# Kernel tuning notes

Measured on AMD Instinct MI355X. Metric: run time of the kernel, lower is better.

The kernel has to match this reference:

```python
import jax, jax.numpy as jnp
import numpy as np

EPS = 1e-06
LAMBDA_PCSL = 0.1
LAMBDA_GPAL = 0.1


def setup_inputs() -> dict:
    key = jax.random.key(0)
    k1, k2 = jax.random.split(key)
    N, D, P = 262144, 256, 512
    features = jax.random.normal(k1, (N, D), dtype=jnp.float32)
    patient_ids = jax.random.randint(k2, (N,), 0, P, dtype=jnp.int64)
    return {"features": features, "patient_ids": patient_ids, "num_patients": P}


def _pafa_loss(features, patient_ids, num_patients):
    # Segmented mean: centroids[p] = mean of features with patient_ids == p
    seg_ids = patient_ids.astype(jnp.int32)
    sums = jax.ops.segment_sum(features, seg_ids, num_segments=num_patients)  # [P, D]
    counts = jax.ops.segment_sum(jnp.ones((features.shape[0],), features.dtype),
                                 seg_ids, num_segments=num_patients)          # [P]
    counts = jnp.maximum(counts, 1.0)  # every patient assumed present (as in original)
    centroids = sums / counts[:, None]                                        # [P, D]

    # Within-patient variance: sum_i ||x_i - c_{pid_i}||^2
    diff = features - centroids[seg_ids]                                      # [N, D]
    within_variance = jnp.sum(diff * diff)

    # Pairwise centroid distances: sum_{i<j} ||c_i - c_j||^2
    #   = P * sum_i ||c_i||^2 - ||sum_i c_i||^2   (exact identity, no O(P^2) loop)
    sq_norms = jnp.sum(centroids * centroids, axis=1)                         # [P]
    total = jnp.sum(centroids, axis=0)                                        # [D]
    P = jnp.asarray(num_patients, centroids.dtype)
    between_distance = P * jnp.sum(sq_norms) - jnp.sum(total * total)

    loss_pcsl = within_variance / (between_distance + EPS)

    # Global patient alignment: mean ||c_p - mean(c)||^2
    global_centroid = jnp.mean(centroids, axis=0)                             # [D]
    gdiff = centroids - global_centroid
    loss_gpal = jnp.mean(jnp.sum(gdiff * gdiff, axis=1))

    return LAMBDA_PCSL * loss_pcsl + LAMBDA_GPAL * loss_gpal


def reference(features, patient_ids, num_patients):
    return _pafa_loss(features, patient_ids, num_patients)
```

## Files before the change

kernel.cpp:

```cpp
#include <hip/hip_runtime.h>


#define DIMS 256
#define NPAT 512
#define HB 64
#define HT 1024
#define CPAD 16


extern "C" __global__ void __launch_bounds__(HT)
k_hist(const int* __restrict__ pids, int N, unsigned* __restrict__ bh)
{
    __shared__ unsigned h[NPAT];
    const int t = threadIdx.x;
    if (t < NPAT) h[t] = 0u;
    __syncthreads();

    const int r = (blockIdx.x * HT + t) * 4;
    if (r + 3 < N) {
        const int4 p4 = *reinterpret_cast<const int4*>(pids + r);
        atomicAdd(&h[p4.x], 1u);
        atomicAdd(&h[p4.y], 1u);
        atomicAdd(&h[p4.z], 1u);
        atomicAdd(&h[p4.w], 1u);
    } else {
        for (int k = 0; k < 4; ++k)
            if (r + k < N) atomicAdd(&h[pids[r + k]], 1u);
    }
    __syncthreads();
    if (t < NPAT) bh[t * HB + blockIdx.x] = h[t];
}

extern "C" __global__ void __launch_bounds__(NPAT)
k_scan(const unsigned* __restrict__ bh, unsigned* __restrict__ counts,
       unsigned* __restrict__ starts, unsigned* __restrict__ cursor,
       float* __restrict__ scalars, float* __restrict__ T)
{
    __shared__ unsigned tmp[NPAT];
    const int t = threadIdx.x;
    unsigned c = 0u;
    const uint4* row = reinterpret_cast<const uint4*>(bh + t * HB);
    #pragma unroll
    for (int k = 0; k < HB / 4; ++k) {
        const uint4 v = row[k];
        c += v.x + v.y + v.z + v.w;
    }
    counts[t] = c;
    tmp[t] = c;
    __syncthreads();
    for (int off = 1; off < NPAT; off <<= 1) {
        const unsigned v = (t >= off) ? tmp[t - off] : 0u;
        __syncthreads();
        tmp[t] += v;
        __syncthreads();
    }
    const unsigned st = tmp[t] - c;
    starts[t] = st;
    cursor[t * CPAD] = st;
    if (t < 4)    scalars[t] = 0.0f;
    if (t < DIMS) T[t]       = 0.0f;
}

extern "C" __global__ void __launch_bounds__(HT)
k_scatter(const int* __restrict__ pids, int N,
          unsigned* __restrict__ cursor, unsigned* __restrict__ idx)
{
    __shared__ unsigned h[NPAT];
    __shared__ unsigned basec[NPAT];
    __shared__ int      spid[HT * 4];

    const int t = threadIdx.x;
    if (t < NPAT) h[t] = 0u;
    __syncthreads();

    const int r = (blockIdx.x * HT + t) * 4;
    int4 p4 = make_int4(-1, -1, -1, -1);
    if (r + 3 < N) {
        p4 = *reinterpret_cast<const int4*>(pids + r);
        atomicAdd(&h[p4.x], 1u);
        atomicAdd(&h[p4.y], 1u);
        atomicAdd(&h[p4.z], 1u);
        atomicAdd(&h[p4.w], 1u);
    } else {
        if (r + 0 < N) { p4.x = pids[r + 0]; atomicAdd(&h[p4.x], 1u); }
        if (r + 1 < N) { p4.y = pids[r + 1]; atomicAdd(&h[p4.y], 1u); }
        if (r + 2 < N) { p4.z = pids[r + 2]; atomicAdd(&h[p4.z], 1u); }
        if (r + 3 < N) { p4.w = pids[r + 3]; atomicAdd(&h[p4.w], 1u); }
    }
    spid[t * 4 + 0] = p4.x;
    spid[t * 4 + 1] = p4.y;
    spid[t * 4 + 2] = p4.z;
    spid[t * 4 + 3] = p4.w;
    __syncthreads();

    if (t < NPAT) {
        const unsigned hc = h[t];
        basec[t] = hc ? atomicAdd(&cursor[t * CPAD], hc) : 0u;
    }
    __syncthreads();

    #pragma unroll
    for (int k = 0; k < 4; ++k) {
        const int pid = spid[t * 4 + k];
        if (pid >= 0) {
            const unsigned pos = atomicAdd(&basec[pid], 1u);
            idx[pos] = (unsigned)(r + k);
        }
    }
}

extern "C" __global__ void __launch_bounds__(512)
k_main(const float* __restrict__ feats, const unsigned* __restrict__ idx,
       const unsigned* __restrict__ counts, const unsigned* __restrict__ starts,
       float* __restrict__ T, float* __restrict__ scalars)
{
    __shared__ float part[8][DIMS];
    __shared__ float sred[8];
    __shared__ float cred[4];

    const int p    = blockIdx.x;
    const int lane = threadIdx.x & 63;
    const int w    = threadIdx.x >> 6;
    const unsigned start = starts[p];
    const unsigned cnt   = counts[p];
    const unsigned base  = lane * 4;

    float ax = 0.f, ay = 0.f, az = 0.f, aw = 0.f;
    float ssq = 0.f;

    unsigned j = (unsigned)w;
    for (; j + 56 < cnt; j += 64) {
        unsigned rr[8];
        #pragma unroll
        for (int k = 0; k < 8; ++k) rr[k] = idx[start + j + 8 * k];
        float4 v[8];
        #pragma unroll
        for (int k = 0; k < 8; ++k)
            v[k] = *reinterpret_cast<const float4*>(feats + (size_t)rr[k] * DIMS + base);
        #pragma unroll
        for (int k = 0; k < 8; ++k) {
            ax += v[k].x; ay += v[k].y; az += v[k].z; aw += v[k].w;
            ssq += v[k].x*v[k].x + v[k].y*v[k].y + v[k].z*v[k].z + v[k].w*v[k].w;
        }
    }
    for (; j < cnt; j += 8) {
        const unsigned row = idx[start + j];
        const float4 v = *reinterpret_cast<const float4*>(feats + (size_t)row * DIMS + base);
        ax += v.x; ay += v.y; az += v.z; aw += v.w;
        ssq += v.x*v.x + v.y*v.y + v.z*v.z + v.w*v.w;
    }

    part[w][base + 0] = ax;
    part[w][base + 1] = ay;
    part[w][base + 2] = az;
    part[w][base + 3] = aw;
    for (int off = 32; off; off >>= 1) ssq += __shfl_down(ssq, off, 64);
    if (lane == 0) sred[w] = ssq;
    __syncthreads();

    const int d = threadIdx.x;
    if (d < DIMS) {
        float s = 0.f;
        #pragma unroll
        for (int ww = 0; ww < 8; ++ww) s += part[ww][d];
        const float cntf = fmaxf((float)cnt, 1.0f);
        const float c = s / cntf;
        atomicAdd(&T[d], c);
        float csq = c * c;
        for (int off = 32; off; off >>= 1) csq += __shfl_down(csq, off, 64);
        if ((d & 63) == 0) cred[d >> 6] = csq;
    }
    __syncthreads();

    if (threadIdx.x == 0) {
        const float s2p = cred[0] + cred[1] + cred[2] + cred[3];
        const float cntf = fmaxf((float)cnt, 1.0f);
        atomicAdd(&scalars[2], s2p);
        atomicAdd(&scalars[1], cntf * s2p);
        float sq = 0.f;
        #pragma unroll
        for (int ww = 0; ww < 8; ++ww) sq += sred[ww];
        atomicAdd(&scalars[0], sq);
    }
}

extern "C" __global__ void __launch_bounds__(DIMS)
k_final(const float* __restrict__ T, const float* __restrict__ scalars,
        const int* __restrict__ nump, float* __restrict__ out)
{
    __shared__ float red[4];
    const int d = threadIdx.x;
    const float t = T[d];
    float tt = t * t;
    for (int off = 32; off; off >>= 1) tt += __shfl_down(tt, off, 64);
    if ((d & 63) == 0) red[d >> 6] = tt;
    __syncthreads();
    if (d == 0) {
        const double TT    = (double)red[0] + red[1] + red[2] + red[3];
        const double SumSq = (double)scalars[0];
        const double S1    = (double)scalars[1];
        const double S2    = (double)scalars[2];
        const double Pd    = (double)(*nump);
        const double within  = SumSq - S1;
        const double between = Pd * S2 - TT;
        const double pcsl = within / (between + 1e-6);
        const double gpal = S2 / Pd - TT / (Pd * Pd);
        out[0] = (float)(0.1 * pcsl + 0.1 * gpal);
    }
}

extern "C" void kernel_launch(void* const* d_in, const int* in_sizes, int n_in,
                              void* d_out, int out_size, void* d_ws, size_t ws_size,
                              hipStream_t stream)
{
    const float* feats = (const float*)d_in[0];
    const int*   pids  = (const int*)d_in[1];
    const int*   nump  = (const int*)d_in[2];
    float*       out   = (float*)d_out;

    const int N = in_sizes[0] / DIMS;

    char* ws = (char*)d_ws;
    unsigned* counts  = (unsigned*)(ws);
    unsigned* starts  = (unsigned*)(ws + 2048);
    float*    scalars = (float*)(ws + 4096);
    float*    T       = (float*)(ws + 4352);
    unsigned* cursor  = (unsigned*)(ws + 8192);
    unsigned* bh      = (unsigned*)(ws + 40960);
    unsigned* idx     = (unsigned*)(ws + 173056);

    k_hist   <<<dim3(HB),   dim3(HT),   0, stream>>>(pids, N, bh);
    k_scan   <<<dim3(1),    dim3(NPAT), 0, stream>>>(bh, counts, starts, cursor,
                                                     scalars, T);
    k_scatter<<<dim3(HB),   dim3(HT),   0, stream>>>(pids, N, cursor, idx);
    k_main   <<<dim3(NPAT), dim3(512),  0, stream>>>(feats, idx, counts, starts,
                                                     T, scalars);
    k_final  <<<dim3(1),    dim3(DIMS), 0, stream>>>(T, scalars, nump, out);
}
```

Before: 76.88 us.

## Precompute per-block scatter offsets, fold final reduction into main kernel, broadcast row indices

The scan kernel now writes an exclusive prefix of each patient's per-block histogram into that histogram. The scatter kernel can then seed its shared cursors directly from starts plus the per-block offset, with no re-histogram and no global atomics on a padded cursor array. The separate final kernel is removed: the last block of k_main, found through an atomic done counter, computes the loss. In k_main, each warp now takes a contiguous chunk of a patient's rows, loads 64 indices in one coalesced read and broadcasts them with readlane. This cuts one launch and redundant scatter work, at the cost of last-block synchronisation and possibly unbalanced chunks.

Result: slower. 207.7 us (+170.2%).

```diff
diff --git a/kernel.cpp b/kernel.cpp
--- a/kernel.cpp
+++ b/kernel.cpp
@@ -5,7 +5,6 @@
 #define NPAT 512
 #define HB 64
 #define HT 1024
-#define CPAD 16
 
 
 extern "C" __global__ void __launch_bounds__(HT)
@@ -32,21 +31,28 @@
 }
 
 extern "C" __global__ void __launch_bounds__(NPAT)
-k_scan(const unsigned* __restrict__ bh, unsigned* __restrict__ counts,
-       unsigned* __restrict__ starts, unsigned* __restrict__ cursor,
-       float* __restrict__ scalars, float* __restrict__ T)
+k_scan(unsigned* __restrict__ bh, unsigned* __restrict__ counts,
+       unsigned* __restrict__ starts, float* __restrict__ scalars,
+       float* __restrict__ T, unsigned* __restrict__ done)
 {
     __shared__ unsigned tmp[NPAT];
     const int t = threadIdx.x;
-    unsigned c = 0u;
-    const uint4* row = reinterpret_cast<const uint4*>(bh + t * HB);
+
+    uint4* row = reinterpret_cast<uint4*>(bh + t * HB);
+    unsigned run = 0u;
     #pragma unroll
     for (int k = 0; k < HB / 4; ++k) {
         const uint4 v = row[k];
-        c += v.x + v.y + v.z + v.w;
-    }
-    counts[t] = c;
-    tmp[t] = c;
+        uint4 e;
+        e.x = run;
+        e.y = e.x + v.x;
+        e.z = e.y + v.y;
+        e.w = e.z + v.z;
+        run = e.w + v.w;
+        row[k] = e;
+    }
+    counts[t] = run;
+    tmp[t] = run;
     __syncthreads();
     for (int off = 1; off < NPAT; off <<= 1) {
         const unsigned v = (t >= off) ? tmp[t - off] : 0u;
@@ -54,69 +60,49 @@
         tmp[t] += v;
         __syncthreads();
     }
-    const unsigned st = tmp[t] - c;
-    starts[t] = st;
-    cursor[t * CPAD] = st;
+    starts[t] = tmp[t] - run;
+
     if (t < 4)    scalars[t] = 0.0f;
+    if (t == 4)   *done      = 0u;
     if (t < DIMS) T[t]       = 0.0f;
 }
 
 extern "C" __global__ void __launch_bounds__(HT)
 k_scatter(const int* __restrict__ pids, int N,
-          unsigned* __restrict__ cursor, unsigned* __restrict__ idx)
-{
-    __shared__ unsigned h[NPAT];
+          const unsigned* __restrict__ bh, const unsigned* __restrict__ starts,
+          unsigned* __restrict__ idx)
+{
     __shared__ unsigned basec[NPAT];
-    __shared__ int      spid[HT * 4];
-
     const int t = threadIdx.x;
-    if (t < NPAT) h[t] = 0u;
+    if (t < NPAT) basec[t] = starts[t] + bh[t * HB + blockIdx.x];
     __syncthreads();
 
     const int r = (blockIdx.x * HT + t) * 4;
-    int4 p4 = make_int4(-1, -1, -1, -1);
     if (r + 3 < N) {
-        p4 = *reinterpret_cast<const int4*>(pids + r);
-        atomicAdd(&h[p4.x], 1u);
-        atomicAdd(&h[p4.y], 1u);
-        atomicAdd(&h[p4.z], 1u);
-        atomicAdd(&h[p4.w], 1u);
+        const int4 p4 = *reinterpret_cast<const int4*>(pids + r);
+        idx[atomicAdd(&basec[p4.x], 1u)] = (unsigned)(r + 0);
+        idx[atomicAdd(&basec[p4.y], 1u)] = (unsigned)(r + 1);
+        idx[atomicAdd(&basec[p4.z], 1u)] = (unsigned)(r + 2);
+        idx[atomicAdd(&basec[p4.w], 1u)] = (unsigned)(r + 3);
     } else {
-        if (r + 0 < N) { p4.x = pids[r + 0]; atomicAdd(&h[p4.x], 1u); }
-        if (r + 1 < N) { p4.y = pids[r + 1]; atomicAdd(&h[p4.y], 1u); }
-        if (r + 2 < N) { p4.z = pids[r + 2]; atomicAdd(&h[p4.z], 1u); }
-        if (r + 3 < N) { p4.w = pids[r + 3]; atomicAdd(&h[p4.w], 1u); }
-    }
-    spid[t * 4 + 0] = p4.x;
-    spid[t * 4 + 1] = p4.y;
-    spid[t * 4 + 2] = p4.z;
-    spid[t * 4 + 3] = p4.w;
-    __syncthreads();
-
-    if (t < NPAT) {
-        const unsigned hc = h[t];
-        basec[t] = hc ? atomicAdd(&cursor[t * CPAD], hc) : 0u;
-    }
-    __syncthreads();
-
-    #pragma unroll
-    for (int k = 0; k < 4; ++k) {
-        const int pid = spid[t * 4 + k];
-        if (pid >= 0) {
-            const unsigned pos = atomicAdd(&basec[pid], 1u);
-            idx[pos] = (unsigned)(r + k);
-        }
+        for (int k = 0; k < 4; ++k)
+            if (r + k < N)
+                idx[atomicAdd(&basec[pids[r + k]], 1u)] = (unsigned)(r + k);
     }
 }
 
 extern "C" __global__ void __launch_bounds__(512)
 k_main(const float* __restrict__ feats, const unsigned* __restrict__ idx,
        const unsigned* __restrict__ counts, const unsigned* __restrict__ starts,
-       float* __restrict__ T, float* __restrict__ scalars)
+       float* __restrict__ T, float* __restrict__ scalars,
+       unsigned* __restrict__ done, const int* __restrict__ nump,
+       float* __restrict__ out)
 {
     __shared__ float part[8][DIMS];
     __shared__ float sred[8];
     __shared__ float cred[4];
+    __shared__ float red[8];
+    __shared__ unsigned lastflag;
 
     const int p    = blockIdx.x;
     const int lane = threadIdx.x & 63;
@@ -128,26 +114,40 @@
     float ax = 0.f, ay = 0.f, az = 0.f, aw = 0.f;
     float ssq = 0.f;
 
-    unsigned j = (unsigned)w;
-    for (; j + 56 < cnt; j += 64) {
-        unsigned rr[8];
-        #pragma unroll
-        for (int k = 0; k < 8; ++k) rr[k] = idx[start + j + 8 * k];
-        float4 v[8];
-        #pragma unroll
-        for (int k = 0; k < 8; ++k)
-            v[k] = *reinterpret_cast<const float4*>(feats + (size_t)rr[k] * DIMS + base);
-        #pragma unroll
-        for (int k = 0; k < 8; ++k) {
-            ax += v[k].x; ay += v[k].y; az += v[k].z; aw += v[k].w;
-            ssq += v[k].x*v[k].x + v[k].y*v[k].y + v[k].z*v[k].z + v[k].w*v[k].w;
+    const unsigned cbeg = start + ((cnt * (unsigned)w) >> 3);
+    const unsigned cend = start + ((cnt * (unsigned)(w + 1)) >> 3);
+
+    for (unsigned g = cbeg; g < cend; g += 64) {
+        const unsigned nr = (cend - g < 64u) ? (cend - g) : 64u;
+        const unsigned myrow = idx[g + lane];
+        if (nr == 64u) {
+            #pragma unroll
+            for (int k0 = 0; k0 < 64; k0 += 8) {
+                float4 v[8];
+                #pragma unroll
+                for (int k = 0; k < 8; ++k) {
+                    const unsigned row =
+                        (unsigned)__builtin_amdgcn_readlane((int)myrow, k0 + k);
+                    v[k] = *reinterpret_cast<const float4*>(
+                        feats + (size_t)row * DIMS + base);
+                }
+                #pragma unroll
+                for (int k = 0; k < 8; ++k) {
+                    ax += v[k].x; ay += v[k].y; az += v[k].z; aw += v[k].w;
+                    ssq += v[k].x*v[k].x + v[k].y*v[k].y
+                         + v[k].z*v[k].z + v[k].w*v[k].w;
+                }
+            }
+        } else {
+            for (unsigned k = 0; k < nr; ++k) {
+                const unsigned row =
+                    (unsigned)__builtin_amdgcn_readlane((int)myrow, (int)k);
+                const float4 v = *reinterpret_cast<const float4*>(
+                    feats + (size_t)row * DIMS + base);
+                ax += v.x; ay += v.y; az += v.z; aw += v.w;
+                ssq += v.x*v.x + v.y*v.y + v.z*v.z + v.w*v.w;
+            }
         }
-    }
-    for (; j < cnt; j += 8) {
-        const unsigned row = idx[start + j];
-        const float4 v = *reinterpret_cast<const float4*>(feats + (size_t)row * DIMS + base);
-        ax += v.x; ay += v.y; az += v.z; aw += v.w;
-        ssq += v.x*v.x + v.y*v.y + v.z*v.z + v.w*v.w;
     }
 
     part[w][base + 0] = ax;
@@ -182,30 +182,39 @@
         for (int ww = 0; ww < 8; ++ww) sq += sred[ww];
         atomicAdd(&scalars[0], sq);
     }
-}
-
-extern "C" __global__ void __launch_bounds__(DIMS)
-k_final(const float* __restrict__ T, const float* __restrict__ scalars,
-        const int* __restrict__ nump, float* __restrict__ out)
-{
-    __shared__ float red[4];
-    const int d = threadIdx.x;
-    const float t = T[d];
-    float tt = t * t;
-    for (int off = 32; off; off >>= 1) tt += __shfl_down(tt, off, 64);
-    if ((d & 63) == 0) red[d >> 6] = tt;
-    __syncthreads();
-    if (d == 0) {
-        const double TT    = (double)red[0] + red[1] + red[2] + red[3];
-        const double SumSq = (double)scalars[0];
-        const double S1    = (double)scalars[1];
-        const double S2    = (double)scalars[2];
-        const double Pd    = (double)(*nump);
-        const double within  = SumSq - S1;
-        const double between = Pd * S2 - TT;
-        const double pcsl = within / (between + 1e-6);
-        const double gpal = S2 / Pd - TT / (Pd * Pd);
-        out[0] = (float)(0.1 * pcsl + 0.1 * gpal);
+
+    __threadfence();
+    if (threadIdx.x == 0) {
+        const unsigned prev = atomicAdd(done, 1u);
+        lastflag = (prev == (unsigned)(gridDim.x - 1)) ? 1u : 0u;
+    }
+    __syncthreads();
+    if (lastflag) {
+        float tt = 0.f;
+        if (d < DIMS) {
+            const float tv = __hip_atomic_load(&T[d], __ATOMIC_RELAXED,
+                                               __HIP_MEMORY_SCOPE_AGENT);
+            tt = tv * tv;
+        }
+        for (int off = 32; off; off >>= 1) tt += __shfl_down(tt, off, 64);
+        if ((d & 63) == 0) red[d >> 6] = tt;
+        __syncthreads();
+        if (d == 0) {
+            const double TT = (double)red[0] + red[1] + red[2] + red[3]
+                            + red[4] + red[5] + red[6] + red[7];
+            const double SumSq = (double)__hip_atomic_load(&scalars[0],
+                __ATOMIC_RELAXED, __HIP_MEMORY_SCOPE_AGENT);
+            const double S1 = (double)__hip_atomic_load(&scalars[1],
+                __ATOMIC_RELAXED, __HIP_MEMORY_SCOPE_AGENT);
+            const double S2 = (double)__hip_atomic_load(&scalars[2],
+                __ATOMIC_RELAXED, __HIP_MEMORY_SCOPE_AGENT);
+            const double Pd = (double)(*nump);
+            const double within  = SumSq - S1;
+            const double between = Pd * S2 - TT;
+            const double pcsl = within / (between + 1e-6);
+            const double gpal = S2 / Pd - TT / (Pd * Pd);
+            out[0] = (float)(0.1 * pcsl + 0.1 * gpal);
+        }
     }
 }
 
@@ -224,16 +233,15 @@
     unsigned* counts  = (unsigned*)(ws);
     unsigned* starts  = (unsigned*)(ws + 2048);
     float*    scalars = (float*)(ws + 4096);
-    float*    T       = (float*)(ws + 4352);
-    unsigned* cursor  = (unsigned*)(ws + 8192);
-    unsigned* bh      = (unsigned*)(ws + 40960);
-    unsigned* idx     = (unsigned*)(ws + 173056);
+    unsigned* done    = (unsigned*)(ws + 4352);
+    float*    T       = (float*)(ws + 4608);
+    unsigned* bh      = (unsigned*)(ws + 8192);
+    unsigned* idx     = (unsigned*)(ws + 139264);
 
     k_hist   <<<dim3(HB),   dim3(HT),   0, stream>>>(pids, N, bh);
-    k_scan   <<<dim3(1),    dim3(NPAT), 0, stream>>>(bh, counts, starts, cursor,
-                                                     scalars, T);
-    k_scatter<<<dim3(HB),   dim3(HT),   0, stream>>>(pids, N, cursor, idx);
+    k_scan   <<<dim3(1),    dim3(NPAT), 0, stream>>>(bh, counts, starts,
+                                                     scalars, T, done);
+    k_scatter<<<dim3(HB),   dim3(HT),   0, stream>>>(pids, N, bh, starts, idx);
     k_main   <<<dim3(NPAT), dim3(512),  0, stream>>>(feats, idx, counts, starts,
-                                                     T, scalars);
-    k_final  <<<dim3(1),    dim3(DIMS), 0, stream>>>(T, scalars, nump, out);
-}
+                                                     T, scalars, done, nump, out);
+}
```
